# Kernel optimization log

Hardware: AMD Instinct MI355X
Metric: run time of the kernel (lower is better)

The kernel has to match this reference:

```python
import math
import jax, jax.numpy as jnp
import numpy as np

N_HEADS = 8
EPS = 1e-6


def setup_inputs() -> dict:
    key = jax.random.key(0)
    k0, k1, k2, k3, k4 = jax.random.split(key, 5)
    B, T, E = 2, 1024, 512
    s = 1.0 / math.sqrt(E)
    x = jax.random.normal(k0, (B, T, E), dtype=jnp.float32)
    w_qkv = jax.random.normal(k1, (3 * E, E), dtype=jnp.float32) * s
    b_qkv = jax.random.normal(k2, (3 * E,), dtype=jnp.float32) * s
    w_out = jax.random.normal(k3, (E, E), dtype=jnp.float32) * s
    b_out = jax.random.normal(k4, (E,), dtype=jnp.float32) * s
    return {"x": x, "w_qkv": w_qkv, "b_qkv": b_qkv, "w_out": w_out, "b_out": b_out}


def reference(x, w_qkv, b_qkv, w_out, b_out):
    B, T, C = x.shape
    H = N_HEADS
    d = C // H

    qkv = x @ w_qkv.T + b_qkv                      # [B,T,3C]
    q, k, v = jnp.split(qkv, 3, axis=-1)

    def to_heads(t):
        return t.reshape(B, T, H, d).transpose(0, 2, 1, 3).astype(jnp.float32)  # [B,H,T,d]

    q, k, v = to_heads(q), to_heads(k), to_heads(v)

    pos = jnp.arange(T, dtype=jnp.float32)
    ang = (math.pi / 2) * pos / T
    cos_w = jnp.cos(ang)[None, None, :, None]      # [1,1,T,1]
    sin_w = jnp.sin(ang)[None, None, :, None]

    q_prime = jax.nn.relu(q)
    k_prime = jax.nn.relu(k)
    q_cos, q_sin = q_prime * cos_w, q_prime * sin_w
    k_cos, k_sin = k_prime * cos_w, k_prime * sin_w

    # causal linear attention via cumulative outer products (cosFormer)
    kv_cos_cs = jnp.cumsum(jnp.einsum('bhtd,bhte->bhtde', k_cos, v), axis=2)
    context = jnp.einsum('bhtd,bhtde->bhte', q_cos, kv_cos_cs)
    kv_sin_cs = jnp.cumsum(jnp.einsum('bhtd,bhte->bhtde', k_sin, v), axis=2)
    context = context + jnp.einsum('bhtd,bhtde->bhte', q_sin, kv_sin_cs)

    norm = (jnp.einsum('bhtd,bhtd->bht', q_cos, jnp.cumsum(k_cos, axis=2))
            + jnp.einsum('bhtd,bhtd->bht', q_sin, jnp.cumsum(k_sin, axis=2)))
    out = context / (norm[..., None] + EPS)        # [B,H,T,d]

    out = out.astype(x.dtype).transpose(0, 2, 1, 3).reshape(B, T, C)
    return out @ w_out.T + b_out
```

## Files before the change

### kernel.cpp

```cpp
#include <hip/hip_runtime.h>

typedef __bf16 bf16_t;
typedef __bf16 bf16x4 __attribute__((ext_vector_type(4)));
typedef __bf16 bf16x8 __attribute__((ext_vector_type(8)));
typedef float f32x4 __attribute__((ext_vector_type(4)));

#define T_SEQ 1024
#define EMB   512
#define NH    8
#define HD    64
#define BATCH 2
#define NBH   (BATCH*NH)
#define CHUNK 64
#define NCHUNK (T_SEQ/CHUNK)
#define NBLK  (NBH*NCHUNK)
#define LDA   72


__global__ __launch_bounds__(256) void cvt3_kernel(
    const float* __restrict__ x, const float* __restrict__ wq,
    const float* __restrict__ wo,
    bf16_t* __restrict__ xb, bf16_t* __restrict__ wqb, bf16_t* __restrict__ wob)
{
    int i = blockIdx.x * 256 + threadIdx.x;
    const float* s; bf16_t* d; int off;
    if (i < 262144)      { s = x;  d = xb;  off = i; }
    else if (i < 458752) { s = wq; d = wqb; off = i - 262144; }
    else                 { s = wo; d = wob; off = i - 458752; }
    float4 v = ((const float4*)s)[off];
    bf16x4 o;
    o[0] = (bf16_t)v.x; o[1] = (bf16_t)v.y;
    o[2] = (bf16_t)v.z; o[3] = (bf16_t)v.w;
    ((bf16x4*)d)[off] = o;
}

__global__ __launch_bounds__(64) void qkv_gemm_kernel(
    const bf16_t* __restrict__ X, const bf16_t* __restrict__ W,
    const float* __restrict__ bias,
    bf16_t* __restrict__ qq, bf16_t* __restrict__ kk, bf16_t* __restrict__ vv)
{
    const int lane = threadIdx.x;
    const int rsel = lane & 15;
    const int koff = (lane >> 4) * 8;
    const int m0 = blockIdx.x * 64;
    const int n0 = blockIdx.y * 64;
    f32x4 acc[4][4] = {};
    const bf16_t* Ap = X + (m0 + rsel) * EMB + koff;
    const bf16_t* Bp = W + (n0 + rsel) * EMB + koff;
#pragma unroll 2
    for (int k0 = 0; k0 < EMB; k0 += 32) {
        bf16x8 af[4], bfr[4];
        for (int i = 0; i < 4; ++i)
            af[i] = *(const bf16x8*)(Ap + i * 16 * EMB + k0);
        for (int j = 0; j < 4; ++j)
            bfr[j] = *(const bf16x8*)(Bp + j * 16 * EMB + k0);
        for (int i = 0; i < 4; ++i)
            for (int j = 0; j < 4; ++j)
                acc[i][j] = __builtin_amdgcn_mfma_f32_16x16x32_bf16(
                    af[i], bfr[j], acc[i][j], 0, 0, 0);
    }
    for (int j = 0; j < 4; ++j) {
        const int n = n0 + j * 16 + rsel;
        const float bn = bias[n];
        const int sec = n >> 9;
        const int c = n & 511;
        const int h = c >> 6, e = c & 63;
        for (int i = 0; i < 4; ++i) {
            const int mb = m0 + i * 16 + (lane >> 4) * 4;
            for (int r = 0; r < 4; ++r) {
                int m = mb + r;
                int b = m >> 10, t = m & 1023;
                float val = acc[i][j][r] + bn;
                int di = ((b * NH + h) * T_SEQ + t) * HD + e;
                if (sec == 0) {
                    qq[di] = (bf16_t)fmaxf(val, 0.f);
                } else if (sec == 1) {
                    kk[di] = (bf16_t)fmaxf(val, 0.f);
                } else {
                    vv[di] = (bf16_t)val;
                }
            }
        }
    }
}

__global__ __launch_bounds__(256) void chunk_sum_kernel(
    const bf16_t* __restrict__ kk, const bf16_t* __restrict__ vv,
    bf16_t* __restrict__ Ssc, bf16_t* __restrict__ Sss,
    float* __restrict__ zc, float* __restrict__ zs)
{
    const int blk = blockIdx.x;
    const int ch = blk & 15;
    __shared__ __align__(16) bf16_t sk[CHUNK * HD];
    __shared__ __align__(16) bf16_t sv[CHUNK * HD];
    __shared__ float cwt[CHUNK], swt[CHUNK];
    const int base = blk * CHUNK * HD;
    for (int i = threadIdx.x; i < CHUNK * HD / 8; i += 256) {
        ((uint4*)sk)[i] = ((const uint4*)(kk + base))[i];
        ((uint4*)sv)[i] = ((const uint4*)(vv + base))[i];
    }
    if (threadIdx.x < CHUNK) {
        int tg = ch * CHUNK + threadIdx.x;
        float ang = 1.5707963267948966f * (float)tg * (1.0f / (float)T_SEQ);
        cwt[threadIdx.x] = cosf(ang);
        swt[threadIdx.x] = sinf(ang);
    }
    __syncthreads();
    const int i  = threadIdx.x & 63;
    const int jg = (threadIdx.x >> 6) * 16;
    float ac[16], as[16];
    for (int jj = 0; jj < 16; ++jj) { ac[jj] = 0.f; as[jj] = 0.f; }
    for (int t = 0; t < CHUNK; ++t) {
        float kv = (float)sk[t * HD + i];
        float kc_ = kv * cwt[t];
        float ks_ = kv * swt[t];
        for (int jj = 0; jj < 16; ++jj) {
            float vj = (float)sv[t * HD + jg + jj];
            ac[jj] += kc_ * vj;
            as[jj] += ks_ * vj;
        }
    }
    bf16_t* oc = Ssc + blk * HD * HD;
    bf16_t* os = Sss + blk * HD * HD;
    for (int jj = 0; jj < 16; ++jj) {
        oc[(jg + jj) * HD + i] = (bf16_t)ac[jj];
        os[(jg + jj) * HD + i] = (bf16_t)as[jj];
    }
    if (threadIdx.x < HD) {
        int ii = threadIdx.x;
        float s = 0.f;
        for (int t = 0; t < CHUNK; ++t) s += (float)sk[t * HD + ii] * cwt[t];
        zc[blk * HD + ii] = s;
    } else if (threadIdx.x < 2 * HD) {
        int ii = threadIdx.x - HD;
        float s = 0.f;
        for (int t = 0; t < CHUNK; ++t) s += (float)sk[t * HD + ii] * swt[t];
        zs[blk * HD + ii] = s;
    }
}

__global__ __launch_bounds__(256) void chunk_out_kernel(
    const bf16_t* __restrict__ qq, const bf16_t* __restrict__ kk,
    const bf16_t* __restrict__ vv,
    const bf16_t* __restrict__ SscT, const bf16_t* __restrict__ SssT,
    const float* __restrict__ zc, const float* __restrict__ zs,
    bf16_t* __restrict__ Y)
{
    const int blk = blockIdx.x;
    const int bh = blk >> 4, ch = blk & 15;
    __shared__ __align__(16) bf16_t sq [CHUNK * LDA];
    __shared__ __align__(16) bf16_t sk [CHUNK * LDA];
    __shared__ __align__(16) bf16_t svT[CHUNK * LDA];
    __shared__ __align__(16) bf16_t sct[CHUNK * LDA];
    __shared__ __align__(16) bf16_t sst[CHUNK * LDA];
    __shared__ __align__(16) bf16_t sp [CHUNK * LDA];
    __shared__ float cwt[CHUNK], swt[CHUNK], cosd[CHUNK];
    __shared__ float zcl[CHUNK], zsl[CHUNK], nrm[CHUNK];

    const int base = blk * CHUNK * HD;
    for (int i = threadIdx.x; i < CHUNK * HD / 8; i += 256) {
        int row = i >> 3, g = i & 7;
        ((uint4*)(sq + row * LDA))[g]  = ((const uint4*)(qq + base))[i];
        ((uint4*)(sk + row * LDA))[g]  = ((const uint4*)(kk + base))[i];
        bf16x8 v8 = *(const bf16x8*)(vv + base + i * 8);
        int t = i >> 3, e0 = (i & 7) * 8;
        for (int j = 0; j < 8; ++j) svT[(e0 + j) * LDA + t] = v8[j];
    }
    {
        const int e0 = threadIdx.x * 16;
        float accC[16], accS[16];
        for (int j = 0; j < 16; ++j) { accC[j] = 0.f; accS[j] = 0.f; }
        const int sb = bh * NCHUNK * HD * HD + e0;
        for (int c = 0; c < ch; ++c) {
            const bf16x8* pc = (const bf16x8*)(SscT + sb + c * HD * HD);
            const bf16x8* ps = (const bf16x8*)(SssT + sb + c * HD * HD);
            bf16x8 c0 = pc[0], c1 = pc[1], s0 = ps[0], s1 = ps[1];
            for (int j = 0; j < 8; ++j) {
                accC[j] += (float)c0[j];  accC[8 + j] += (float)c1[j];
                accS[j] += (float)s0[j];  accS[8 + j] += (float)s1[j];
            }
        }
        const int row = threadIdx.x >> 2, col = (threadIdx.x & 3) * 16;
        bf16x8 oc0, oc1, os0, os1;
        for (int j = 0; j < 8; ++j) {
            oc0[j] = (bf16_t)accC[j];  oc1[j] = (bf16_t)accC[8 + j];
            os0[j] = (bf16_t)accS[j];  os1[j] = (bf16_t)accS[8 + j];
        }
        *(bf16x8*)(sct + row * LDA + col) = oc0;
        *(bf16x8*)(sct + row * LDA + col + 8) = oc1;
        *(bf16x8*)(sst + row * LDA + col) = os0;
        *(bf16x8*)(sst + row * LDA + col + 8) = os1;
    }
    if (threadIdx.x < HD) {
        int tl = threadIdx.x;
        float s = 0.f;
        for (int c = 0; c < ch; ++c) s += zc[(bh * NCHUNK + c) * HD + tl];
        zcl[tl] = s;
        int tg = ch * CHUNK + tl;
        float angg = 1.5707963267948966f * (float)tg * (1.0f / (float)T_SEQ);
        cwt[tl] = cosf(angg);
        swt[tl] = sinf(angg);
        cosd[tl] = cosf(1.5707963267948966f * (float)tl * (1.0f / (float)T_SEQ));
    } else if (threadIdx.x < 2 * HD) {
        int i = threadIdx.x - HD;
        float s = 0.f;
        for (int c = 0; c < ch; ++c) s += zs[(bh * NCHUNK + c) * HD + i];
        zsl[i] = s;
    }
    __syncthreads();

    const int w = threadIdx.x >> 6;
    const int lane = threadIdx.x & 63;
    const int rsel = lane & 15;
    const int koff = (lane >> 4) * 8;
    const int myrow = w * 16 + rsel;

    bf16x8 aq0 = *(const bf16x8*)(sq + myrow * LDA + koff);
    bf16x8 aq1 = *(const bf16x8*)(sq + myrow * LDA + koff + 32);
    for (int nt = 0; nt < 4; ++nt) {
        const int n0 = nt * 16;
        f32x4 pacc = {0.f, 0.f, 0.f, 0.f};
        bf16x8 b0 = *(const bf16x8*)(sk + (n0 + rsel) * LDA + koff);
        bf16x8 b1 = *(const bf16x8*)(sk + (n0 + rsel) * LDA + koff + 32);
        pacc = __builtin_amdgcn_mfma_f32_16x16x32_bf16(aq0, b0, pacc, 0, 0, 0);
        pacc = __builtin_amdgcn_mfma_f32_16x16x32_bf16(aq1, b1, pacc, 0, 0, 0);
        const int s = n0 + (lane & 15);
        const int tb = w * 16 + (lane >> 4) * 4;
        for (int r = 0; r < 4; ++r) {
            int t = tb + r;
            float p = (s <= t) ? pacc[r] * cosd[t - s] : 0.f;
            sp[t * LDA + s] = (bf16_t)p;
        }
    }

    if (lane < 16) {
        int row = w * 16 + lane;
        float nv = 0.f;
        const bf16x8* pr = (const bf16x8*)(sp + row * LDA);
        for (int g = 0; g < 8; ++g) {
            bf16x8 pv = pr[g];
            for (int j = 0; j < 8; ++j) nv += (float)pv[j];
        }
        float cwr = cwt[row], swr = swt[row];
        const bf16x8* qr = (const bf16x8*)(sq + row * LDA);
        for (int g = 0; g < 8; ++g) {
            bf16x8 qv = qr[g];
            for (int j = 0; j < 8; ++j)
                nv += (float)qv[j] * (cwr * zcl[g * 8 + j] + swr * zsl[g * 8 + j]);
        }
        nrm[row] = nv;
    }

    const float cwq = cwt[myrow], swq = swt[myrow];
    bf16x8 qc0, qc1, qs0, qs1;
    for (int j = 0; j < 8; ++j) {
        qc0[j] = (bf16_t)((float)aq0[j] * cwq);
        qc1[j] = (bf16_t)((float)aq1[j] * cwq);
        qs0[j] = (bf16_t)((float)aq0[j] * swq);
        qs1[j] = (bf16_t)((float)aq1[j] * swq);
    }
    bf16x8 ap0 = *(const bf16x8*)(sp + myrow * LDA + koff);
    bf16x8 ap1 = *(const bf16x8*)(sp + myrow * LDA + koff + 32);

    const int b = bh >> 3, h = bh & 7;
    for (int nt = 0; nt < 4; ++nt) {
        const int n0 = nt * 16;
        const bf16_t* bvp = svT + (n0 + rsel) * LDA + koff;
        const bf16_t* bcp = sct + (n0 + rsel) * LDA + koff;
        const bf16_t* bsp = sst + (n0 + rsel) * LDA + koff;
        f32x4 acc = {0.f, 0.f, 0.f, 0.f};
        acc = __builtin_amdgcn_mfma_f32_16x16x32_bf16(ap0, *(const bf16x8*)(bvp), acc, 0, 0, 0);
        acc = __builtin_amdgcn_mfma_f32_16x16x32_bf16(ap1, *(const bf16x8*)(bvp + 32), acc, 0, 0, 0);
        acc = __builtin_amdgcn_mfma_f32_16x16x32_bf16(qc0, *(const bf16x8*)(bcp), acc, 0, 0, 0);
        acc = __builtin_amdgcn_mfma_f32_16x16x32_bf16(qc1, *(const bf16x8*)(bcp + 32), acc, 0, 0, 0);
        acc = __builtin_amdgcn_mfma_f32_16x16x32_bf16(qs0, *(const bf16x8*)(bsp), acc, 0, 0, 0);
        acc = __builtin_amdgcn_mfma_f32_16x16x32_bf16(qs1, *(const bf16x8*)(bsp + 32), acc, 0, 0, 0);
        const int col = n0 + (lane & 15);
        const int tb = w * 16 + (lane >> 4) * 4;
        for (int r = 0; r < 4; ++r) {
            int row = tb + r;
            float inv = 1.0f / (nrm[row] + 1e-6f);
            int tg = ch * CHUNK + row;
            Y[((b * T_SEQ + tg) * EMB) + h * HD + col] = (bf16_t)(acc[r] * inv);
        }
    }
}

__global__ __launch_bounds__(256) void out_gemm_kernel(
    const bf16_t* __restrict__ Yb, const bf16_t* __restrict__ W,
    const float* __restrict__ bias, float* __restrict__ out)
{
    const int w = threadIdx.x >> 6;
    const int lane = threadIdx.x & 63;
    const int rsel = lane & 15;
    const int koff = (lane >> 4) * 8;
    const int m0 = blockIdx.x * 64 + (w & 1) * 32;
    const int n0 = blockIdx.y * 64 + (w >> 1) * 32;
    f32x4 acc[2][2] = {};
    const bf16_t* Ap = Yb + (m0 + rsel) * EMB + koff;
    const bf16_t* Bp = W + (n0 + rsel) * EMB + koff;
#pragma unroll 4
    for (int k0 = 0; k0 < EMB; k0 += 32) {
        bf16x8 af[2], bfr[2];
        for (int i = 0; i < 2; ++i)
            af[i] = *(const bf16x8*)(Ap + i * 16 * EMB + k0);
        for (int j = 0; j < 2; ++j)
            bfr[j] = *(const bf16x8*)(Bp + j * 16 * EMB + k0);
        for (int i = 0; i < 2; ++i)
            for (int j = 0; j < 2; ++j)
                acc[i][j] = __builtin_amdgcn_mfma_f32_16x16x32_bf16(
                    af[i], bfr[j], acc[i][j], 0, 0, 0);
    }
    for (int j = 0; j < 2; ++j) {
        const int n = n0 + j * 16 + rsel;
        const float bn = bias[n];
        for (int i = 0; i < 2; ++i) {
            const int mb = m0 + i * 16 + (lane >> 4) * 4;
            for (int r = 0; r < 4; ++r)
                out[(mb + r) * EMB + n] = acc[i][j][r] + bn;
        }
    }
}

extern "C" void kernel_launch(void* const* d_in, const int* in_sizes, int n_in,
                              void* d_out, int out_size, void* d_ws, size_t ws_size,
                              hipStream_t stream) {
    const float* x     = (const float*)d_in[0];
    const float* w_qkv = (const float*)d_in[1];
    const float* b_qkv = (const float*)d_in[2];
    const float* w_out = (const float*)d_in[3];
    const float* b_out = (const float*)d_in[4];
    float* out = (float*)d_out;

    char* w = (char*)d_ws;
    const size_t N_X   = (size_t)BATCH * T_SEQ * EMB;
    const size_t N_WQ  = (size_t)3 * EMB * EMB;
    const size_t N_WO  = (size_t)EMB * EMB;
    bf16_t* xb   = (bf16_t*)w;                 w += N_X  * sizeof(bf16_t);
    bf16_t* wqb  = (bf16_t*)w;                 w += N_WQ * sizeof(bf16_t);
    bf16_t* wob  = (bf16_t*)w;                 w += N_WO * sizeof(bf16_t);
    const size_t SZ_BHTD = (size_t)NBH * T_SEQ * HD * sizeof(bf16_t);
    bf16_t* qq = (bf16_t*)w;                   w += SZ_BHTD;
    bf16_t* kk = (bf16_t*)w;                   w += SZ_BHTD;
    bf16_t* vv = (bf16_t*)w;                   w += SZ_BHTD;
    bf16_t* Y  = (bf16_t*)w;                   w += SZ_BHTD;
    bf16_t* SscT = (bf16_t*)w;                 w += (size_t)NBLK * HD * HD * sizeof(bf16_t);
    bf16_t* SssT = (bf16_t*)w;                 w += (size_t)NBLK * HD * HD * sizeof(bf16_t);
    float* zc = (float*)w;                     w += (size_t)NBLK * HD * sizeof(float);
    float* zs = (float*)w;

    cvt3_kernel<<<2048, 256, 0, stream>>>(x, w_qkv, w_out, xb, wqb, wob);
    qkv_gemm_kernel<<<dim3(2048 / 64, 1536 / 64), 64, 0, stream>>>(
        xb, wqb, b_qkv, qq, kk, vv);
    chunk_sum_kernel<<<NBLK, 256, 0, stream>>>(kk, vv, SscT, SssT, zc, zs);
    chunk_out_kernel<<<NBLK, 256, 0, stream>>>(qq, kk, vv, SscT, SssT, zc, zs, Y);
    out_gemm_kernel<<<dim3(2048 / 64, 512 / 64), 256, 0, stream>>>(
        Y, w_out != nullptr ? wob : wob, b_out, out);
}
```

Baseline: 124.2 us.

## Fuse all five stages into one cooperative persistent kernel with grid syncs

Replaces the five separate launches (convert, QKV GEMM, chunk sums, chunk output, output GEMM) with a single cooperative kernel of 256 blocks that separates the stages with grid-wide barriers. The goal is to remove launch gaps and per-kernel tail overhead. In exchange, each stage is constrained to 256 blocks: the QKV GEMM uses only 3 of 4 waves per block, and grid.sync has its own cost. The old multi-kernel path is kept as a fallback if the cooperative launch fails.

New measurement: 241.7 us. 1.95x slower.

```diff
diff --git a/kernel.cpp b/kernel.cpp
--- a/kernel.cpp
+++ b/kernel.cpp
@@ -1,4 +1,7 @@
 #include <hip/hip_runtime.h>
+#include <hip/hip_cooperative_groups.h>
+
+namespace cg = cooperative_groups;
 
 typedef __bf16 bf16_t;
 typedef __bf16 bf16x4 __attribute__((ext_vector_type(4)));
@@ -15,7 +18,332 @@
 #define NCHUNK (T_SEQ/CHUNK)
 #define NBLK  (NBH*NCHUNK)
 #define LDA   72
-
+#define N_X   (BATCH*T_SEQ*EMB)
+#define N_WQ  (3*EMB*EMB)
+#define N_WO  (EMB*EMB)
+#define NTD   (NBH*T_SEQ*HD)
+
+
+__global__ __launch_bounds__(256) void fused_kernel(
+    const float* __restrict__ x, const float* __restrict__ wq32,
+    const float* __restrict__ bq, const float* __restrict__ wo32,
+    const float* __restrict__ bo, float* __restrict__ out,
+    char* __restrict__ ws)
+{
+    bf16_t* xb  = (bf16_t*)ws;
+    bf16_t* wqb = xb + N_X;
+    bf16_t* wob = wqb + N_WQ;
+    bf16_t* qq  = wob + N_WO;
+    bf16_t* kk  = qq + NTD;
+    bf16_t* vv  = kk + NTD;
+    bf16_t* Y   = vv + NTD;
+    bf16_t* SscT = Y + NTD;
+    bf16_t* SssT = SscT + (size_t)NBLK * HD * HD;
+    float* zc = (float*)(SssT + (size_t)NBLK * HD * HD);
+    float* zs = zc + (size_t)NBLK * HD;
+
+    __shared__ __align__(16) bf16_t s_a[CHUNK * LDA];
+    __shared__ __align__(16) bf16_t s_b[CHUNK * LDA];
+    __shared__ __align__(16) bf16_t s_c[CHUNK * LDA];
+    __shared__ __align__(16) bf16_t s_d[CHUNK * LDA];
+    __shared__ __align__(16) bf16_t s_e[CHUNK * LDA];
+    __shared__ __align__(16) bf16_t s_f[CHUNK * LDA];
+    __shared__ float f_a[CHUNK], f_b[CHUNK], f_c[CHUNK];
+    __shared__ float f_d[CHUNK], f_e[CHUNK], f_f[CHUNK];
+
+    cg::grid_group grid = cg::this_grid();
+    const int blk = blockIdx.x;
+
+    {
+        const int tid = blk * 256 + threadIdx.x;
+        for (int i = tid; i < 524288; i += 65536) {
+            const float* s; bf16_t* d; int off;
+            if (i < 262144)      { s = x;    d = xb;  off = i; }
+            else if (i < 458752) { s = wq32; d = wqb; off = i - 262144; }
+            else                 { s = wo32; d = wob; off = i - 458752; }
+            float4 v = ((const float4*)s)[off];
+            bf16x4 o;
+            o[0] = (bf16_t)v.x; o[1] = (bf16_t)v.y;
+            o[2] = (bf16_t)v.z; o[3] = (bf16_t)v.w;
+            ((bf16x4*)d)[off] = o;
+        }
+    }
+    grid.sync();
+
+    {
+        const int w = threadIdx.x >> 6;
+        const int lane = threadIdx.x & 63;
+        if (w < 3) {
+            const int gt = blk * 3 + w;
+            const int m0 = (gt & 31) * 64;
+            const int n0 = (gt >> 5) * 64;
+            const int rsel = lane & 15;
+            const int koff = (lane >> 4) * 8;
+            f32x4 acc[4][4] = {};
+            const bf16_t* Ap = xb + (m0 + rsel) * EMB + koff;
+            const bf16_t* Bp = wqb + (n0 + rsel) * EMB + koff;
+#pragma unroll 2
+            for (int k0 = 0; k0 < EMB; k0 += 32) {
+                bf16x8 af[4], bfr[4];
+                for (int i = 0; i < 4; ++i)
+                    af[i] = *(const bf16x8*)(Ap + i * 16 * EMB + k0);
+                for (int j = 0; j < 4; ++j)
+                    bfr[j] = *(const bf16x8*)(Bp + j * 16 * EMB + k0);
+                for (int i = 0; i < 4; ++i)
+                    for (int j = 0; j < 4; ++j)
+                        acc[i][j] = __builtin_amdgcn_mfma_f32_16x16x32_bf16(
+                            af[i], bfr[j], acc[i][j], 0, 0, 0);
+            }
+            for (int j = 0; j < 4; ++j) {
+                const int n = n0 + j * 16 + rsel;
+                const float bn = bq[n];
+                const int sec = n >> 9;
+                const int c = n & 511;
+                const int h = c >> 6, e = c & 63;
+                for (int i = 0; i < 4; ++i) {
+                    const int mb = m0 + i * 16 + (lane >> 4) * 4;
+                    for (int r = 0; r < 4; ++r) {
+                        int m = mb + r;
+                        int b = m >> 10, t = m & 1023;
+                        float val = acc[i][j][r] + bn;
+                        int di = ((b * NH + h) * T_SEQ + t) * HD + e;
+                        if (sec == 0) {
+                            qq[di] = (bf16_t)fmaxf(val, 0.f);
+                        } else if (sec == 1) {
+                            kk[di] = (bf16_t)fmaxf(val, 0.f);
+                        } else {
+                            vv[di] = (bf16_t)val;
+                        }
+                    }
+                }
+            }
+        }
+    }
+    grid.sync();
+
+    {
+        const int ch = blk & 15;
+        bf16_t* sk = s_a;
+        bf16_t* sv = s_b;
+        float* cwt = f_a; float* swt = f_b;
+        const int base = blk * CHUNK * HD;
+        for (int i = threadIdx.x; i < CHUNK * HD / 8; i += 256) {
+            ((uint4*)sk)[i] = ((const uint4*)(kk + base))[i];
+            ((uint4*)sv)[i] = ((const uint4*)(vv + base))[i];
+        }
+        if (threadIdx.x < CHUNK) {
+            int tg = ch * CHUNK + threadIdx.x;
+            float ang = 1.5707963267948966f * (float)tg * (1.0f / (float)T_SEQ);
+            cwt[threadIdx.x] = cosf(ang);
+            swt[threadIdx.x] = sinf(ang);
+        }
+        __syncthreads();
+        const int i  = threadIdx.x & 63;
+        const int jg = (threadIdx.x >> 6) * 16;
+        float ac[16], as[16];
+        for (int jj = 0; jj < 16; ++jj) { ac[jj] = 0.f; as[jj] = 0.f; }
+        for (int t = 0; t < CHUNK; ++t) {
+            float kv = (float)sk[t * HD + i];
+            float kc_ = kv * cwt[t];
+            float ks_ = kv * swt[t];
+            for (int jj = 0; jj < 16; ++jj) {
+                float vj = (float)sv[t * HD + jg + jj];
+                ac[jj] += kc_ * vj;
+                as[jj] += ks_ * vj;
+            }
+        }
+        bf16_t* oc = SscT + blk * HD * HD;
+        bf16_t* os = SssT + blk * HD * HD;
+        for (int jj = 0; jj < 16; ++jj) {
+            oc[(jg + jj) * HD + i] = (bf16_t)ac[jj];
+            os[(jg + jj) * HD + i] = (bf16_t)as[jj];
+        }
+        if (threadIdx.x < HD) {
+            int ii = threadIdx.x;
+            float s = 0.f;
+            for (int t = 0; t < CHUNK; ++t) s += (float)sk[t * HD + ii] * cwt[t];
+            zc[blk * HD + ii] = s;
+        } else if (threadIdx.x < 2 * HD) {
+            int ii = threadIdx.x - HD;
+            float s = 0.f;
+            for (int t = 0; t < CHUNK; ++t) s += (float)sk[t * HD + ii] * swt[t];
+            zs[blk * HD + ii] = s;
+        }
+    }
+    grid.sync();
+
+    {
+        const int bh = blk >> 4, ch = blk & 15;
+        bf16_t* sq = s_a;  bf16_t* sk = s_b;  bf16_t* svT = s_c;
+        bf16_t* sct = s_d; bf16_t* sst = s_e; bf16_t* sp  = s_f;
+        float* cwt = f_a; float* swt = f_b; float* cosd = f_c;
+        float* zcl = f_d; float* zsl = f_e; float* nrm = f_f;
+
+        const int base = blk * CHUNK * HD;
+        for (int i = threadIdx.x; i < CHUNK * HD / 8; i += 256) {
+            int row = i >> 3, g = i & 7;
+            ((uint4*)(sq + row * LDA))[g]  = ((const uint4*)(qq + base))[i];
+            ((uint4*)(sk + row * LDA))[g]  = ((const uint4*)(kk + base))[i];
+            bf16x8 v8 = *(const bf16x8*)(vv + base + i * 8);
+            int t = i >> 3, e0 = (i & 7) * 8;
+            for (int j = 0; j < 8; ++j) svT[(e0 + j) * LDA + t] = v8[j];
+        }
+        {
+            const int e0 = threadIdx.x * 16;
+            float accC[16], accS[16];
+            for (int j = 0; j < 16; ++j) { accC[j] = 0.f; accS[j] = 0.f; }
+            const int sb = bh * NCHUNK * HD * HD + e0;
+            for (int c = 0; c < ch; ++c) {
+                const bf16x8* pc = (const bf16x8*)(SscT + sb + c * HD * HD);
+                const bf16x8* ps = (const bf16x8*)(SssT + sb + c * HD * HD);
+                bf16x8 c0 = pc[0], c1 = pc[1], s0 = ps[0], s1 = ps[1];
+                for (int j = 0; j < 8; ++j) {
+                    accC[j] += (float)c0[j];  accC[8 + j] += (float)c1[j];
+                    accS[j] += (float)s0[j];  accS[8 + j] += (float)s1[j];
+                }
+            }
+            const int row = threadIdx.x >> 2, col = (threadIdx.x & 3) * 16;
+            bf16x8 oc0, oc1, os0, os1;
+            for (int j = 0; j < 8; ++j) {
+                oc0[j] = (bf16_t)accC[j];  oc1[j] = (bf16_t)accC[8 + j];
+                os0[j] = (bf16_t)accS[j];  os1[j] = (bf16_t)accS[8 + j];
+            }
+            *(bf16x8*)(sct + row * LDA + col) = oc0;
+            *(bf16x8*)(sct + row * LDA + col + 8) = oc1;
+            *(bf16x8*)(sst + row * LDA + col) = os0;
+            *(bf16x8*)(sst + row * LDA + col + 8) = os1;
+        }
+        if (threadIdx.x < HD) {
+            int tl = threadIdx.x;
+            float s = 0.f;
+            for (int c = 0; c < ch; ++c) s += zc[(bh * NCHUNK + c) * HD + tl];
+            zcl[tl] = s;
+            int tg = ch * CHUNK + tl;
+            float angg = 1.5707963267948966f * (float)tg * (1.0f / (float)T_SEQ);
+            cwt[tl] = cosf(angg);
+            swt[tl] = sinf(angg);
+            cosd[tl] = cosf(1.5707963267948966f * (float)tl * (1.0f / (float)T_SEQ));
+        } else if (threadIdx.x < 2 * HD) {
+            int i = threadIdx.x - HD;
+            float s = 0.f;
+            for (int c = 0; c < ch; ++c) s += zs[(bh * NCHUNK + c) * HD + i];
+            zsl[i] = s;
+        }
+        __syncthreads();
+
+        const int w = threadIdx.x >> 6;
+        const int lane = threadIdx.x & 63;
+        const int rsel = lane & 15;
+        const int koff = (lane >> 4) * 8;
+        const int myrow = w * 16 + rsel;
+
+        bf16x8 aq0 = *(const bf16x8*)(sq + myrow * LDA + koff);
+        bf16x8 aq1 = *(const bf16x8*)(sq + myrow * LDA + koff + 32);
+        for (int nt = 0; nt < 4; ++nt) {
+            const int n0 = nt * 16;
+            f32x4 pacc = {0.f, 0.f, 0.f, 0.f};
+            bf16x8 b0 = *(const bf16x8*)(sk + (n0 + rsel) * LDA + koff);
+            bf16x8 b1 = *(const bf16x8*)(sk + (n0 + rsel) * LDA + koff + 32);
+            pacc = __builtin_amdgcn_mfma_f32_16x16x32_bf16(aq0, b0, pacc, 0, 0, 0);
+            pacc = __builtin_amdgcn_mfma_f32_16x16x32_bf16(aq1, b1, pacc, 0, 0, 0);
+            const int s = n0 + (lane & 15);
+            const int tb = w * 16 + (lane >> 4) * 4;
+            for (int r = 0; r < 4; ++r) {
+                int t = tb + r;
+                float p = (s <= t) ? pacc[r] * cosd[t - s] : 0.f;
+                sp[t * LDA + s] = (bf16_t)p;
+            }
+        }
+
+        if (lane < 16) {
+            int row = w * 16 + lane;
+            float nv = 0.f;
+            const bf16x8* pr = (const bf16x8*)(sp + row * LDA);
+            for (int g = 0; g < 8; ++g) {
+                bf16x8 pv = pr[g];
+                for (int j = 0; j < 8; ++j) nv += (float)pv[j];
+            }
+            float cwr = cwt[row], swr = swt[row];
+            const bf16x8* qr = (const bf16x8*)(sq + row * LDA);
+            for (int g = 0; g < 8; ++g) {
+                bf16x8 qv = qr[g];
+                for (int j = 0; j < 8; ++j)
+                    nv += (float)qv[j] * (cwr * zcl[g * 8 + j] + swr * zsl[g * 8 + j]);
+            }
+            nrm[row] = nv;
+        }
+
+        const float cwq = cwt[myrow], swq = swt[myrow];
+        bf16x8 qc0, qc1, qs0, qs1;
+        for (int j = 0; j < 8; ++j) {
+            qc0[j] = (bf16_t)((float)aq0[j] * cwq);
+            qc1[j] = (bf16_t)((float)aq1[j] * cwq);
+            qs0[j] = (bf16_t)((float)aq0[j] * swq);
+            qs1[j] = (bf16_t)((float)aq1[j] * swq);
+        }
+        bf16x8 ap0 = *(const bf16x8*)(sp + myrow * LDA + koff);
+        bf16x8 ap1 = *(const bf16x8*)(sp + myrow * LDA + koff + 32);
+
+        __syncthreads();
+
+        const int b = bh >> 3, h = bh & 7;
+        for (int nt = 0; nt < 4; ++nt) {
+            const int n0 = nt * 16;
+            const bf16_t* bvp = svT + (n0 + rsel) * LDA + koff;
+            const bf16_t* bcp = sct + (n0 + rsel) * LDA + koff;
+            const bf16_t* bsp = sst + (n0 + rsel) * LDA + koff;
+            f32x4 acc = {0.f, 0.f, 0.f, 0.f};
+            acc = __builtin_amdgcn_mfma_f32_16x16x32_bf16(ap0, *(const bf16x8*)(bvp), acc, 0, 0, 0);
+            acc = __builtin_amdgcn_mfma_f32_16x16x32_bf16(ap1, *(const bf16x8*)(bvp + 32), acc, 0, 0, 0);
+            acc = __builtin_amdgcn_mfma_f32_16x16x32_bf16(qc0, *(const bf16x8*)(bcp), acc, 0, 0, 0);
+            acc = __builtin_amdgcn_mfma_f32_16x16x32_bf16(qc1, *(const bf16x8*)(bcp + 32), acc, 0, 0, 0);
+            acc = __builtin_amdgcn_mfma_f32_16x16x32_bf16(qs0, *(const bf16x8*)(bsp), acc, 0, 0, 0);
+            acc = __builtin_amdgcn_mfma_f32_16x16x32_bf16(qs1, *(const bf16x8*)(bsp + 32), acc, 0, 0, 0);
+            const int col = n0 + (lane & 15);
+            const int tb = w * 16 + (lane >> 4) * 4;
+            for (int r = 0; r < 4; ++r) {
+                int row = tb + r;
+                float inv = 1.0f / (nrm[row] + 1e-6f);
+                int tg = ch * CHUNK + row;
+                Y[((b * T_SEQ + tg) * EMB) + h * HD + col] = (bf16_t)(acc[r] * inv);
+            }
+        }
+    }
+    grid.sync();
+
+    {
+        const int w = threadIdx.x >> 6;
+        const int lane = threadIdx.x & 63;
+        const int rsel = lane & 15;
+        const int koff = (lane >> 4) * 8;
+        const int m0 = (blk & 31) * 64 + (w & 1) * 32;
+        const int n0 = (blk >> 5) * 64 + (w >> 1) * 32;
+        f32x4 acc[2][2] = {};
+        const bf16_t* Ap = Y + (m0 + rsel) * EMB + koff;
+        const bf16_t* Bp = wob + (n0 + rsel) * EMB + koff;
+#pragma unroll 4
+        for (int k0 = 0; k0 < EMB; k0 += 32) {
+            bf16x8 af[2], bfr[2];
+            for (int i = 0; i < 2; ++i)
+                af[i] = *(const bf16x8*)(Ap + i * 16 * EMB + k0);
+            for (int j = 0; j < 2; ++j)
+                bfr[j] = *(const bf16x8*)(Bp + j * 16 * EMB + k0);
+            for (int i = 0; i < 2; ++i)
+                for (int j = 0; j < 2; ++j)
+                    acc[i][j] = __builtin_amdgcn_mfma_f32_16x16x32_bf16(
+                        af[i], bfr[j], acc[i][j], 0, 0, 0);
+        }
+        for (int j = 0; j < 2; ++j) {
+            const int n = n0 + j * 16 + rsel;
+            const float bn = bo[n];
+            for (int i = 0; i < 2; ++i) {
+                const int mb = m0 + i * 16 + (lane >> 4) * 4;
+                for (int r = 0; r < 4; ++r)
+                    out[(mb + r) * EMB + n] = acc[i][j][r] + bn;
+            }
+        }
+    }
+}
 
 __global__ __launch_bounds__(256) void cvt3_kernel(
     const float* __restrict__ x, const float* __restrict__ wq,
@@ -331,15 +659,22 @@
     const float* w_out = (const float*)d_in[3];
     const float* b_out = (const float*)d_in[4];
     float* out = (float*)d_out;
-
-    char* w = (char*)d_ws;
-    const size_t N_X   = (size_t)BATCH * T_SEQ * EMB;
-    const size_t N_WQ  = (size_t)3 * EMB * EMB;
-    const size_t N_WO  = (size_t)EMB * EMB;
-    bf16_t* xb   = (bf16_t*)w;                 w += N_X  * sizeof(bf16_t);
-    bf16_t* wqb  = (bf16_t*)w;                 w += N_WQ * sizeof(bf16_t);
-    bf16_t* wob  = (bf16_t*)w;                 w += N_WO * sizeof(bf16_t);
-    const size_t SZ_BHTD = (size_t)NBH * T_SEQ * HD * sizeof(bf16_t);
+    char* wsb = (char*)d_ws;
+
+    void* params[7] = {
+        (void*)&x, (void*)&w_qkv, (void*)&b_qkv, (void*)&w_out,
+        (void*)&b_out, (void*)&out, (void*)&wsb
+    };
+    hipError_t err = hipLaunchCooperativeKernel(
+        (const void*)fused_kernel, dim3(256), dim3(256), params, 0, stream);
+    if (err == hipSuccess) return;
+    (void)hipGetLastError();
+
+    char* w = wsb;
+    bf16_t* xb   = (bf16_t*)w;                 w += (size_t)N_X  * sizeof(bf16_t);
+    bf16_t* wqb  = (bf16_t*)w;                 w += (size_t)N_WQ * sizeof(bf16_t);
+    bf16_t* wob  = (bf16_t*)w;                 w += (size_t)N_WO * sizeof(bf16_t);
+    const size_t SZ_BHTD = (size_t)NTD * sizeof(bf16_t);
     bf16_t* qq = (bf16_t*)w;                   w += SZ_BHTD;
     bf16_t* kk = (bf16_t*)w;                   w += SZ_BHTD;
     bf16_t* vv = (bf16_t*)w;                   w += SZ_BHTD;
@@ -355,5 +690,5 @@
     chunk_sum_kernel<<<NBLK, 256, 0, stream>>>(kk, vv, SscT, SssT, zc, zs);
     chunk_out_kernel<<<NBLK, 256, 0, stream>>>(qq, kk, vv, SscT, SssT, zc, zs, Y);
     out_gemm_kernel<<<dim3(2048 / 64, 512 / 64), 256, 0, stream>>>(
-        Y, w_out != nullptr ? wob : wob, b_out, out);
+        Y, wob, b_out, out);
 }
```

## Fuse chunk-sum into chunk-out, recomputing prefix states with MFMA per block

Applied to the files above, without the earlier changes.

Removes the separate chunk_sum kernel and its global state buffers. Each chunk_out block now recomputes the prefix KV states for all earlier chunks itself, using MFMA outer-product accumulation in registers, and accumulates the normalizer sums from shared memory. This saves a kernel launch and the global round trip for the states, but adds redundant work that grows linearly with chunk index, leaving late chunks with up to 15 chunk loads and extra syncs.

Result: slower. 139.9 us (+12.7%).

```diff
diff --git a/kernel.cpp b/kernel.cpp
--- a/kernel.cpp
+++ b/kernel.cpp
@@ -84,67 +84,9 @@
     }
 }
 
-__global__ __launch_bounds__(256) void chunk_sum_kernel(
-    const bf16_t* __restrict__ kk, const bf16_t* __restrict__ vv,
-    bf16_t* __restrict__ Ssc, bf16_t* __restrict__ Sss,
-    float* __restrict__ zc, float* __restrict__ zs)
-{
-    const int blk = blockIdx.x;
-    const int ch = blk & 15;
-    __shared__ __align__(16) bf16_t sk[CHUNK * HD];
-    __shared__ __align__(16) bf16_t sv[CHUNK * HD];
-    __shared__ float cwt[CHUNK], swt[CHUNK];
-    const int base = blk * CHUNK * HD;
-    for (int i = threadIdx.x; i < CHUNK * HD / 8; i += 256) {
-        ((uint4*)sk)[i] = ((const uint4*)(kk + base))[i];
-        ((uint4*)sv)[i] = ((const uint4*)(vv + base))[i];
-    }
-    if (threadIdx.x < CHUNK) {
-        int tg = ch * CHUNK + threadIdx.x;
-        float ang = 1.5707963267948966f * (float)tg * (1.0f / (float)T_SEQ);
-        cwt[threadIdx.x] = cosf(ang);
-        swt[threadIdx.x] = sinf(ang);
-    }
-    __syncthreads();
-    const int i  = threadIdx.x & 63;
-    const int jg = (threadIdx.x >> 6) * 16;
-    float ac[16], as[16];
-    for (int jj = 0; jj < 16; ++jj) { ac[jj] = 0.f; as[jj] = 0.f; }
-    for (int t = 0; t < CHUNK; ++t) {
-        float kv = (float)sk[t * HD + i];
-        float kc_ = kv * cwt[t];
-        float ks_ = kv * swt[t];
-        for (int jj = 0; jj < 16; ++jj) {
-            float vj = (float)sv[t * HD + jg + jj];
-            ac[jj] += kc_ * vj;
-            as[jj] += ks_ * vj;
-        }
-    }
-    bf16_t* oc = Ssc + blk * HD * HD;
-    bf16_t* os = Sss + blk * HD * HD;
-    for (int jj = 0; jj < 16; ++jj) {
-        oc[(jg + jj) * HD + i] = (bf16_t)ac[jj];
-        os[(jg + jj) * HD + i] = (bf16_t)as[jj];
-    }
-    if (threadIdx.x < HD) {
-        int ii = threadIdx.x;
-        float s = 0.f;
-        for (int t = 0; t < CHUNK; ++t) s += (float)sk[t * HD + ii] * cwt[t];
-        zc[blk * HD + ii] = s;
-    } else if (threadIdx.x < 2 * HD) {
-        int ii = threadIdx.x - HD;
-        float s = 0.f;
-        for (int t = 0; t < CHUNK; ++t) s += (float)sk[t * HD + ii] * swt[t];
-        zs[blk * HD + ii] = s;
-    }
-}
-
 __global__ __launch_bounds__(256) void chunk_out_kernel(
     const bf16_t* __restrict__ qq, const bf16_t* __restrict__ kk,
-    const bf16_t* __restrict__ vv,
-    const bf16_t* __restrict__ SscT, const bf16_t* __restrict__ SssT,
-    const float* __restrict__ zc, const float* __restrict__ zs,
-    bf16_t* __restrict__ Y)
+    const bf16_t* __restrict__ vv, bf16_t* __restrict__ Y)
 {
     const int blk = blockIdx.x;
     const int bh = blk >> 4, ch = blk & 15;
@@ -166,55 +108,77 @@
         int t = i >> 3, e0 = (i & 7) * 8;
         for (int j = 0; j < 8; ++j) svT[(e0 + j) * LDA + t] = v8[j];
     }
-    {
-        const int e0 = threadIdx.x * 16;
-        float accC[16], accS[16];
-        for (int j = 0; j < 16; ++j) { accC[j] = 0.f; accS[j] = 0.f; }
-        const int sb = bh * NCHUNK * HD * HD + e0;
-        for (int c = 0; c < ch; ++c) {
-            const bf16x8* pc = (const bf16x8*)(SscT + sb + c * HD * HD);
-            const bf16x8* ps = (const bf16x8*)(SssT + sb + c * HD * HD);
-            bf16x8 c0 = pc[0], c1 = pc[1], s0 = ps[0], s1 = ps[1];
-            for (int j = 0; j < 8; ++j) {
-                accC[j] += (float)c0[j];  accC[8 + j] += (float)c1[j];
-                accS[j] += (float)s0[j];  accS[8 + j] += (float)s1[j];
-            }
-        }
-        const int row = threadIdx.x >> 2, col = (threadIdx.x & 3) * 16;
-        bf16x8 oc0, oc1, os0, os1;
-        for (int j = 0; j < 8; ++j) {
-            oc0[j] = (bf16_t)accC[j];  oc1[j] = (bf16_t)accC[8 + j];
-            os0[j] = (bf16_t)accS[j];  os1[j] = (bf16_t)accS[8 + j];
-        }
-        *(bf16x8*)(sct + row * LDA + col) = oc0;
-        *(bf16x8*)(sct + row * LDA + col + 8) = oc1;
-        *(bf16x8*)(sst + row * LDA + col) = os0;
-        *(bf16x8*)(sst + row * LDA + col + 8) = os1;
-    }
-    if (threadIdx.x < HD) {
+    if (threadIdx.x < CHUNK) {
         int tl = threadIdx.x;
-        float s = 0.f;
-        for (int c = 0; c < ch; ++c) s += zc[(bh * NCHUNK + c) * HD + tl];
-        zcl[tl] = s;
         int tg = ch * CHUNK + tl;
         float angg = 1.5707963267948966f * (float)tg * (1.0f / (float)T_SEQ);
         cwt[tl] = cosf(angg);
         swt[tl] = sinf(angg);
         cosd[tl] = cosf(1.5707963267948966f * (float)tl * (1.0f / (float)T_SEQ));
-    } else if (threadIdx.x < 2 * HD) {
-        int i = threadIdx.x - HD;
-        float s = 0.f;
-        for (int c = 0; c < ch; ++c) s += zs[(bh * NCHUNK + c) * HD + i];
-        zsl[i] = s;
-    }
-    __syncthreads();
+    }
 
     const int w = threadIdx.x >> 6;
     const int lane = threadIdx.x & 63;
     const int rsel = lane & 15;
     const int koff = (lane >> 4) * 8;
+
+    f32x4 pacC[4] = {};
+    f32x4 pacS[4] = {};
+    float zacc = 0.f;
+    for (int c = 0; c < ch; ++c) {
+        const int cb = (bh * NCHUNK + c) * CHUNK * HD;
+        for (int i = threadIdx.x; i < CHUNK * HD / 8; i += 256) {
+            int t = i >> 3, i0 = (i & 7) * 8;
+            float ang = 1.5707963267948966f * (float)(c * CHUNK + t) * (1.0f / (float)T_SEQ);
+            float cw = cosf(ang), sw = sinf(ang);
+            bf16x8 k8 = *(const bf16x8*)(kk + cb + i * 8);
+            bf16x8 v8 = *(const bf16x8*)(vv + cb + i * 8);
+            for (int j = 0; j < 8; ++j) {
+                float kf = (float)k8[j];
+                sct[(i0 + j) * LDA + t] = (bf16_t)(kf * cw);
+                sst[(i0 + j) * LDA + t] = (bf16_t)(kf * sw);
+                sp [(i0 + j) * LDA + t] = v8[j];
+            }
+        }
+        __syncthreads();
+        bf16x8 a0 = *(const bf16x8*)(sp + (w * 16 + rsel) * LDA + koff);
+        bf16x8 a1 = *(const bf16x8*)(sp + (w * 16 + rsel) * LDA + koff + 32);
+        for (int nt = 0; nt < 4; ++nt) {
+            const bf16_t* bc = sct + (nt * 16 + rsel) * LDA + koff;
+            const bf16_t* bs = sst + (nt * 16 + rsel) * LDA + koff;
+            pacC[nt] = __builtin_amdgcn_mfma_f32_16x16x32_bf16(a0, *(const bf16x8*)(bc), pacC[nt], 0, 0, 0);
+            pacC[nt] = __builtin_amdgcn_mfma_f32_16x16x32_bf16(a1, *(const bf16x8*)(bc + 32), pacC[nt], 0, 0, 0);
+            pacS[nt] = __builtin_amdgcn_mfma_f32_16x16x32_bf16(a0, *(const bf16x8*)(bs), pacS[nt], 0, 0, 0);
+            pacS[nt] = __builtin_amdgcn_mfma_f32_16x16x32_bf16(a1, *(const bf16x8*)(bs + 32), pacS[nt], 0, 0, 0);
+        }
+        if (threadIdx.x < HD) {
+            const bf16x8* pr = (const bf16x8*)(sct + threadIdx.x * LDA);
+            for (int g = 0; g < 8; ++g) {
+                bf16x8 v8 = pr[g];
+                for (int j = 0; j < 8; ++j) zacc += (float)v8[j];
+            }
+        } else if (threadIdx.x < 2 * HD) {
+            const bf16x8* pr = (const bf16x8*)(sst + (threadIdx.x - HD) * LDA);
+            for (int g = 0; g < 8; ++g) {
+                bf16x8 v8 = pr[g];
+                for (int j = 0; j < 8; ++j) zacc += (float)v8[j];
+            }
+        }
+        __syncthreads();
+    }
+    for (int nt = 0; nt < 4; ++nt) {
+        const int i = nt * 16 + rsel;
+        const int eb = w * 16 + (lane >> 4) * 4;
+        for (int r = 0; r < 4; ++r) {
+            sct[(eb + r) * LDA + i] = (bf16_t)pacC[nt][r];
+            sst[(eb + r) * LDA + i] = (bf16_t)pacS[nt][r];
+        }
+    }
+    if (threadIdx.x < HD)          zcl[threadIdx.x] = zacc;
+    else if (threadIdx.x < 2 * HD) zsl[threadIdx.x - HD] = zacc;
+    __syncthreads();
+
     const int myrow = w * 16 + rsel;
-
     bf16x8 aq0 = *(const bf16x8*)(sq + myrow * LDA + koff);
     bf16x8 aq1 = *(const bf16x8*)(sq + myrow * LDA + koff + 32);
     for (int nt = 0; nt < 4; ++nt) {
@@ -343,17 +307,12 @@
     bf16_t* qq = (bf16_t*)w;                   w += SZ_BHTD;
     bf16_t* kk = (bf16_t*)w;                   w += SZ_BHTD;
     bf16_t* vv = (bf16_t*)w;                   w += SZ_BHTD;
-    bf16_t* Y  = (bf16_t*)w;                   w += SZ_BHTD;
-    bf16_t* SscT = (bf16_t*)w;                 w += (size_t)NBLK * HD * HD * sizeof(bf16_t);
-    bf16_t* SssT = (bf16_t*)w;                 w += (size_t)NBLK * HD * HD * sizeof(bf16_t);
-    float* zc = (float*)w;                     w += (size_t)NBLK * HD * sizeof(float);
-    float* zs = (float*)w;
+    bf16_t* Y  = (bf16_t*)w;
 
     cvt3_kernel<<<2048, 256, 0, stream>>>(x, w_qkv, w_out, xb, wqb, wob);
     qkv_gemm_kernel<<<dim3(2048 / 64, 1536 / 64), 64, 0, stream>>>(
         xb, wqb, b_qkv, qq, kk, vv);
-    chunk_sum_kernel<<<NBLK, 256, 0, stream>>>(kk, vv, SscT, SssT, zc, zs);
-    chunk_out_kernel<<<NBLK, 256, 0, stream>>>(qq, kk, vv, SscT, SssT, zc, zs, Y);
+    chunk_out_kernel<<<NBLK, 256, 0, stream>>>(qq, kk, vv, Y);
     out_gemm_kernel<<<dim3(2048 / 64, 512 / 64), 256, 0, stream>>>(
-        Y, w_out != nullptr ? wob : wob, b_out, out);
-}
+        Y, wob, b_out, out);
+}
```
